# Optimization experiments

Hardware: AMD Instinct MI355X
Metric: run time of the kernel (lower is better)

## Reference

```python
import jax, jax.numpy as jnp
import numpy as np

H = 16   # num_heads
K = 2    # top_k experts per token


def _layer_norm(x, g, b, eps=1e-5):
    mu = jnp.mean(x, axis=-1, keepdims=True)
    var = jnp.mean(jnp.square(x - mu), axis=-1, keepdims=True)
    return (x - mu) * jax.lax.rsqrt(var + eps) * g + b


def setup_inputs() -> dict:
    key = jax.random.key(0)
    ks = jax.random.split(key, 8)
    B, S, D, E = 2, 2048, 1024, 8
    sc = 0.02
    return {
        "x": jax.random.normal(ks[0], (B, S, D), jnp.float32),
        "wq": jax.random.normal(ks[1], (D, D), jnp.float32) * sc,
        "wk": jax.random.normal(ks[2], (D, D), jnp.float32) * sc,
        "wv": jax.random.normal(ks[3], (D, D), jnp.float32) * sc,
        "wo": jax.random.normal(ks[4], (D, D), jnp.float32) * sc,
        "ln1_g": jnp.ones((D,), jnp.float32),
        "ln1_b": jnp.zeros((D,), jnp.float32),
        "ln2_g": jnp.ones((D,), jnp.float32),
        "ln2_b": jnp.zeros((D,), jnp.float32),
        "router_w": jax.random.normal(ks[5], (E, D), jnp.float32) * sc,
        "expert_w": jax.random.normal(ks[6], (E, D, D), jnp.float32) * sc,
    }


def reference(x, wq, wk, wv, wo, ln1_g, ln1_b, ln2_g, ln2_b, router_w, expert_w):
    B, S, D = x.shape
    E = expert_w.shape[0]
    hd = D // H

    # ---- attention sublayer: x = x + attn(norm1(x)) ----
    h = _layer_norm(x, ln1_g, ln1_b)
    q = (h @ wq.T).reshape(B, S, H, hd).transpose(0, 2, 1, 3)  # bhsd
    k = (h @ wk.T).reshape(B, S, H, hd).transpose(0, 2, 1, 3)
    v = (h @ wv.T).reshape(B, S, H, hd).transpose(0, 2, 1, 3)
    scores = jnp.einsum("bhqd,bhkd->bhqk", q, k) / jnp.sqrt(jnp.float32(hd))
    causal = jnp.tril(jnp.ones((S, S), dtype=bool))
    scores = jnp.where(causal, scores, jnp.finfo(scores.dtype).min)
    probs = jax.nn.softmax(scores, axis=-1)
    attn = jnp.einsum("bhqk,bhkd->bhqd", probs, v)
    attn = attn.transpose(0, 2, 1, 3).reshape(B, S, D) @ wo.T
    x = x + attn

    # ---- MoE sublayer: x = x + moe(norm2(x)) ----
    h2 = _layer_norm(x, ln2_g, ln2_b)
    logits = jnp.einsum("bsd,ed->bse", h2, router_w)          # [B,S,E]
    top_logits, top_ids = jax.lax.top_k(logits, K)            # [B,S,K]
    gates = jax.nn.softmax(top_logits, axis=-1)               # [B,S,K]
    # dense combine weights over experts (E is small): sum_k gate_k * onehot(id_k)
    combine = jnp.sum(jax.nn.one_hot(top_ids, E, dtype=h2.dtype) * gates[..., None], axis=-2)  # [B,S,E]
    # per-token matvec with expert weights: token @ W_e.T for each expert, then weighted sum
    y = jnp.einsum("bsd,eod->bseo", h2, expert_w)             # [B,S,E,D]
    moe_out = jnp.einsum("bse,bseo->bso", combine, y)
    return x + moe_out
```

## Files before the change

kernel.cpp:

```cpp
#include <hip/hip_runtime.h>
#include <hip/hip_bf16.h>
#include <cstdint>


typedef __bf16 bf16;
typedef __bf16 bf16x8 __attribute__((ext_vector_type(8)));
typedef __bf16 bf16x4 __attribute__((ext_vector_type(4)));
typedef float f32x4 __attribute__((ext_vector_type(4)));
typedef float f32x16 __attribute__((ext_vector_type(16)));

#define MFMA(a, b, c) __builtin_amdgcn_mfma_f32_16x16x32_bf16(a, b, c, 0, 0, 0)
#define MFMA32(a, b, c) __builtin_amdgcn_mfma_f32_32x32x16_bf16(a, b, c, 0, 0, 0)

__device__ __forceinline__ void gld16(void* lds, const void* g) {
  __builtin_amdgcn_global_load_lds(
      (const __attribute__((address_space(1))) void*)g,
      (__attribute__((address_space(3))) void*)lds, 16, 0, 0);
}

__global__ void prep_weights(const float* __restrict__ wq, const float* __restrict__ wk,
                             const float* __restrict__ wv, const float* __restrict__ wo,
                             const float* __restrict__ expw,
                             bf16* __restrict__ wqh, bf16* __restrict__ wql,
                             bf16* __restrict__ wkh, bf16* __restrict__ wkl,
                             bf16* __restrict__ wvh,
                             bf16* __restrict__ woh, bf16* __restrict__ wol,
                             bf16* __restrict__ ewh) {
  int bid = blockIdx.x;
  if (bid < 4096) {
    int wsel = bid >> 10;
    const float* src = wsel == 0 ? wq : wsel == 1 ? wk : wsel == 2 ? wv : wo;
    bf16* hi = wsel == 0 ? wqh : wsel == 1 ? wkh : wsel == 2 ? wvh : woh;
    bf16* lo = wsel == 0 ? wql : wsel == 1 ? wkl : wsel == 2 ? (bf16*)nullptr : wol;
    int i = ((bid & 1023) * 256 + threadIdx.x) * 4;
    float4 v = *(const float4*)(src + i);
    float a[4] = {v.x, v.y, v.z, v.w};
#pragma unroll
    for (int j = 0; j < 4; j++) {
      bf16 h = (bf16)a[j];
      hi[i + j] = h;
      if (wsel != 2) lo[i + j] = (bf16)(a[j] - (float)h);
    }
  } else {
    int i = ((bid - 4096) * 256 + threadIdx.x) * 4;
    float4 v = *(const float4*)(expw + i);
    ewh[i] = (bf16)v.x; ewh[i + 1] = (bf16)v.y;
    ewh[i + 2] = (bf16)v.z; ewh[i + 3] = (bf16)v.w;
  }
}

__global__ void ln_split(const float* __restrict__ x, const float* __restrict__ g,
                         const float* __restrict__ b, bf16* __restrict__ hi,
                         bf16* __restrict__ lo) {
  int tok = blockIdx.x, t = threadIdx.x;
  float4 v = ((const float4*)(x + (size_t)tok * 1024))[t];
  float s = v.x + v.y + v.z + v.w;
  float ss = v.x * v.x + v.y * v.y + v.z * v.z + v.w * v.w;
#pragma unroll
  for (int o = 1; o < 64; o <<= 1) { s += __shfl_xor(s, o); ss += __shfl_xor(ss, o); }
  __shared__ float red[8];
  int w = t >> 6, lane = t & 63;
  if (lane == 0) { red[w] = s; red[4 + w] = ss; }
  __syncthreads();
  s = red[0] + red[1] + red[2] + red[3];
  ss = red[4] + red[5] + red[6] + red[7];
  float mu = s * (1.f / 1024.f);
  float rstd = rsqrtf(ss * (1.f / 1024.f) - mu * mu + 1e-5f);
  float4 gv = ((const float4*)g)[t], bv = ((const float4*)b)[t];
  float y[4] = {(v.x - mu) * rstd * gv.x + bv.x, (v.y - mu) * rstd * gv.y + bv.y,
                (v.z - mu) * rstd * gv.z + bv.z, (v.w - mu) * rstd * gv.w + bv.w};
  size_t o = (size_t)tok * 1024 + t * 4;
#pragma unroll
  for (int j = 0; j < 4; j++) {
    bf16 h = (bf16)y[j];
    hi[o + j] = h;
    lo[o + j] = (bf16)(y[j] - (float)h);
  }
}

__global__ void ln2route(const float* __restrict__ x0,
                         const float* __restrict__ P0, const float* __restrict__ P1,
                         const float* __restrict__ g, const float* __restrict__ b,
                         const float* __restrict__ rw, float* __restrict__ outp,
                         bf16* __restrict__ h2h, int* __restrict__ eid,
                         float2* __restrict__ gout) {
  int tok = blockIdx.x, t = threadIdx.x;
  float4 xv = ((const float4*)(x0 + (size_t)tok * 1024))[t];
  float4 p0 = ((const float4*)(P0 + (size_t)tok * 1024))[t];
  float4 p1 = ((const float4*)(P1 + (size_t)tok * 1024))[t];
  float4 v;
  v.x = xv.x + p0.x + p1.x;
  v.y = xv.y + p0.y + p1.y;
  v.z = xv.z + p0.z + p1.z;
  v.w = xv.w + p0.w + p1.w;
  ((float4*)(outp + (size_t)tok * 1024))[t] = v;
  float s = v.x + v.y + v.z + v.w;
  float ss = v.x * v.x + v.y * v.y + v.z * v.z + v.w * v.w;
#pragma unroll
  for (int o = 1; o < 64; o <<= 1) { s += __shfl_xor(s, o); ss += __shfl_xor(ss, o); }
  __shared__ float red[8];
  __shared__ float h2s[1024];
  __shared__ float lg[8];
  int w = t >> 6, lane = t & 63;
  if (lane == 0) { red[w] = s; red[4 + w] = ss; }
  __syncthreads();
  s = red[0] + red[1] + red[2] + red[3];
  ss = red[4] + red[5] + red[6] + red[7];
  float mu = s * (1.f / 1024.f);
  float rstd = rsqrtf(ss * (1.f / 1024.f) - mu * mu + 1e-5f);
  float4 gv = ((const float4*)g)[t], bv = ((const float4*)b)[t];
  float4 y;
  y.x = (v.x - mu) * rstd * gv.x + bv.x;
  y.y = (v.y - mu) * rstd * gv.y + bv.y;
  y.z = (v.z - mu) * rstd * gv.z + bv.z;
  y.w = (v.w - mu) * rstd * gv.w + bv.w;
  ((float4*)h2s)[t] = y;
  size_t o = (size_t)tok * 1024 + t * 4;
  h2h[o] = (bf16)y.x; h2h[o + 1] = (bf16)y.y;
  h2h[o + 2] = (bf16)y.z; h2h[o + 3] = (bf16)y.w;
  __syncthreads();
  float a0 = 0.f, a1 = 0.f;
  const float4* r0 = (const float4*)(rw + (2 * w) * 1024);
  const float4* r1 = (const float4*)(rw + (2 * w + 1) * 1024);
#pragma unroll
  for (int it = 0; it < 4; it++) {
    float4 xv2 = ((const float4*)h2s)[lane + 64 * it];
    float4 w0 = r0[lane + 64 * it];
    float4 w1 = r1[lane + 64 * it];
    a0 += xv2.x * w0.x + xv2.y * w0.y + xv2.z * w0.z + xv2.w * w0.w;
    a1 += xv2.x * w1.x + xv2.y * w1.y + xv2.z * w1.z + xv2.w * w1.w;
  }
#pragma unroll
  for (int o2 = 1; o2 < 64; o2 <<= 1) {
    a0 += __shfl_xor(a0, o2);
    a1 += __shfl_xor(a1, o2);
  }
  if (lane == 0) { lg[2 * w] = a0; lg[2 * w + 1] = a1; }
  __syncthreads();
  if (t == 0) {
    int i0 = 0; float l0 = lg[0];
#pragma unroll
    for (int e = 1; e < 8; e++) if (lg[e] > l0) { l0 = lg[e]; i0 = e; }
    int i1 = -1; float l1 = -3e38f;
#pragma unroll
    for (int e = 0; e < 8; e++) if (e != i0 && lg[e] > l1) { l1 = lg[e]; i1 = e; }
    float e1 = __expf(l1 - l0);
    float den = 1.f + e1;
    eid[tok] = i0 | (i1 << 4);
    gout[tok] = make_float2(1.f / den, e1 / den);
  }
}

__global__ void build_lists(const int* __restrict__ eid,
                            const float2* __restrict__ gv,
                            int* __restrict__ tlist, float* __restrict__ glist,
                            int* __restrict__ cnt) {
  int e = blockIdx.x, t = threadIdx.x;
  int lane = t & 63, w = t >> 6;
  __shared__ int wt[4];
  int base = 0;
  for (int c = 0; c < 16; c++) {
    int tok = c * 256 + t;
    int pair = eid[tok];
    int e0 = pair & 15, e1 = pair >> 4;
    bool p = (e0 == e) || (e1 == e);
    float2 g2 = gv[tok];
    float gate = (e0 == e) ? g2.x : g2.y;
    unsigned long long m = __ballot(p);
    int rank = __popcll(m & ((1ull << lane) - 1ull));
    if (lane == 0) wt[w] = __popcll(m);
    __syncthreads();
    int off = base;
    for (int i = 0; i < w; i++) off += wt[i];
    if (p) {
      tlist[e * 4096 + off + rank] = tok;
      glist[e * 4096 + off + rank] = gate;
    }
    base += wt[0] + wt[1] + wt[2] + wt[3];
    __syncthreads();
  }
  if (t == 0) cnt[e] = base;
  int pad = (base + 127) & ~127;
  if (pad > 4096) pad = 4096;
  for (int i = base + t; i < pad; i += 256) {
    tlist[e * 4096 + i] = 0;
    glist[e * 4096 + i] = 0.f;
  }
}

__device__ __forceinline__ void gemm_core_split(
    const bf16* __restrict__ Ah, const bf16* __restrict__ Al,
    const bf16* __restrict__ Bh, const bf16* __restrict__ Bl, int m0, int n0,
    f32x4 (&acc)[4][4]) {
  __shared__ __align__(16) bf16 As_h[4096], As_l[4096], Bs_h[4096], Bs_l[4096];
  int t = threadIdx.x, lane = t & 63, w = t >> 6;
  int i0 = t, i1 = t + 256;
  const bf16* a0h = Ah + (size_t)(m0 + (i0 >> 2)) * 1024 + (i0 & 3) * 8;
  const bf16* a1h = Ah + (size_t)(m0 + (i1 >> 2)) * 1024 + (i1 & 3) * 8;
  const bf16* a0l = Al + (size_t)(m0 + (i0 >> 2)) * 1024 + (i0 & 3) * 8;
  const bf16* a1l = Al + (size_t)(m0 + (i1 >> 2)) * 1024 + (i1 & 3) * 8;
  const bf16* b0h = Bh + (size_t)(n0 + (i0 >> 2)) * 1024 + (i0 & 3) * 8;
  const bf16* b1h = Bh + (size_t)(n0 + (i1 >> 2)) * 1024 + (i1 & 3) * 8;
  const bf16* b0l = Bl + (size_t)(n0 + (i0 >> 2)) * 1024 + (i0 & 3) * 8;
  const bf16* b1l = Bl + (size_t)(n0 + (i1 >> 2)) * 1024 + (i1 & 3) * 8;
  int wm = (w >> 1) * 64, wn = (w & 1) * 64;
  int lr = lane & 15, lq = lane >> 4;
  for (int k0 = 0; k0 < 1024; k0 += 32) {
    __syncthreads();
    gld16(&As_h[i0 * 8], a0h + k0); gld16(&As_h[i1 * 8], a1h + k0);
    gld16(&As_l[i0 * 8], a0l + k0); gld16(&As_l[i1 * 8], a1l + k0);
    gld16(&Bs_h[i0 * 8], b0h + k0); gld16(&Bs_h[i1 * 8], b1h + k0);
    gld16(&Bs_l[i0 * 8], b0l + k0); gld16(&Bs_l[i1 * 8], b1l + k0);
    __syncthreads();
    bf16x8 ah[4], al4[4], bh[4], bl4[4];
#pragma unroll
    for (int i = 0; i < 4; i++) {
      ah[i]  = *(const bf16x8*)&As_h[(wm + i * 16 + lr) * 32 + lq * 8];
      al4[i] = *(const bf16x8*)&As_l[(wm + i * 16 + lr) * 32 + lq * 8];
      bh[i]  = *(const bf16x8*)&Bs_h[(wn + i * 16 + lr) * 32 + lq * 8];
      bl4[i] = *(const bf16x8*)&Bs_l[(wn + i * 16 + lr) * 32 + lq * 8];
    }
#pragma unroll
    for (int i = 0; i < 4; i++)
#pragma unroll
      for (int j = 0; j < 4; j++) {
        f32x4 c = acc[i][j];
        c = MFMA(ah[i], bh[j], c);
        c = MFMA(ah[i], bl4[j], c);
        c = MFMA(al4[i], bh[j], c);
        acc[i][j] = c;
      }
  }
}

__global__ __launch_bounds__(256, 3) void gemm_qkv(
    const bf16* __restrict__ hh, const bf16* __restrict__ hl,
    const bf16* __restrict__ wqh, const bf16* __restrict__ wql,
    const bf16* __restrict__ wkh, const bf16* __restrict__ wkl,
    const bf16* __restrict__ wvh,
    bf16* __restrict__ qh, bf16* __restrict__ ql, bf16* __restrict__ kh,
    bf16* __restrict__ kl, bf16* __restrict__ vth) {
  int n0 = blockIdx.x * 128, m0 = blockIdx.y * 128, z = blockIdx.z;
  int t = threadIdx.x, lane = t & 63, w = t >> 6;
  int wm = (w >> 1) * 64, wn = (w & 1) * 64, lr = lane & 15, lq = lane >> 4;
  if (z < 2) {
    const bf16* Bh = z ? wkh : wqh;
    const bf16* Bl = z ? wkl : wql;
    f32x4 acc[4][4];
#pragma unroll
    for (int i = 0; i < 4; i++)
#pragma unroll
      for (int j = 0; j < 4; j++) acc[i][j] = (f32x4){0.f, 0.f, 0.f, 0.f};
    gemm_core_split(hh, hl, Bh, Bl, m0, n0, acc);
    bf16* Oh = z ? kh : qh;
    bf16* Ol = z ? kl : ql;
    float scale = z ? 1.0f : (0.125f * 1.44269504f);
#pragma unroll
    for (int i = 0; i < 4; i++)
#pragma unroll
      for (int j = 0; j < 4; j++)
#pragma unroll
        for (int r = 0; r < 4; r++) {
          size_t row = m0 + wm + i * 16 + lq * 4 + r;
          int col = n0 + wn + j * 16 + lr;
          float v = acc[i][j][r] * scale;
          bf16 h = (bf16)v;
          Oh[row * 1024 + col] = h;
          Ol[row * 1024 + col] = (bf16)(v - (float)h);
        }
  } else {
    __shared__ __align__(16) bf16 As[4096], Bs[4096];
    int i0 = t, i1 = t + 256;
    const bf16* a0 = hh + (size_t)(m0 + (i0 >> 2)) * 1024 + (i0 & 3) * 8;
    const bf16* a1 = hh + (size_t)(m0 + (i1 >> 2)) * 1024 + (i1 & 3) * 8;
    const bf16* b0 = wvh + (size_t)(n0 + (i0 >> 2)) * 1024 + (i0 & 3) * 8;
    const bf16* b1 = wvh + (size_t)(n0 + (i1 >> 2)) * 1024 + (i1 & 3) * 8;
    f32x4 acc[4][4];
#pragma unroll
    for (int i = 0; i < 4; i++)
#pragma unroll
      for (int j = 0; j < 4; j++) acc[i][j] = (f32x4){0.f, 0.f, 0.f, 0.f};
    for (int k0 = 0; k0 < 1024; k0 += 32) {
      __syncthreads();
      gld16(&As[i0 * 8], a0 + k0); gld16(&As[i1 * 8], a1 + k0);
      gld16(&Bs[i0 * 8], b0 + k0); gld16(&Bs[i1 * 8], b1 + k0);
      __syncthreads();
      bf16x8 af[4], bfr[4];
#pragma unroll
      for (int i = 0; i < 4; i++) {
        af[i] = *(const bf16x8*)&As[(wm + i * 16 + lr) * 32 + lq * 8];
        bfr[i] = *(const bf16x8*)&Bs[(wn + i * 16 + lr) * 32 + lq * 8];
      }
#pragma unroll
      for (int i = 0; i < 4; i++)
#pragma unroll
        for (int j = 0; j < 4; j++) acc[i][j] = MFMA(af[i], bfr[j], acc[i][j]);
    }
    int bb = m0 >> 11;
    int srow0 = m0 & 2047;
#pragma unroll
    for (int i = 0; i < 4; i++)
#pragma unroll
      for (int j = 0; j < 4; j++) {
        int col = n0 + wn + j * 16 + lr;
        int head = col >> 6, d = col & 63;
        int s = srow0 + wm + i * 16 + lq * 4;
        int ss = (s & ~63) | (((((s >> 2) & 15)) ^ (d & 15)) << 2);
        bf16x4 hv;
#pragma unroll
        for (int r = 0; r < 4; r++) hv[r] = (bf16)acc[i][j][r];
        size_t off = ((size_t)((bb * 16 + head) * 64 + d)) * 2048 + ss;
        *(bf16x4*)(vth + off) = hv;
      }
  }
}

__global__ __launch_bounds__(256, 2) void gemm_wo(
    const float* __restrict__ Oacc, const float* __restrict__ Lacc,
    const bf16* __restrict__ bh, const bf16* __restrict__ bl,
    float* __restrict__ P0, float* __restrict__ P1) {
  int n0 = blockIdx.x * 128, m0 = blockIdx.y * 128, z = blockIdx.z;
  float* P = z ? P1 : P0;
  int kb = z * 512;
  __shared__ __align__(16) bf16 As_h[4096], As_l[4096], Bs_h[4096], Bs_l[4096];
  int t = threadIdx.x, lane = t & 63, w = t >> 6;
  int i0 = t, i1 = t + 256;
  int row0 = m0 + (i0 >> 2), row1 = m0 + (i1 >> 2);
  const float* a0 = Oacc + (size_t)row0 * 1024 + (i0 & 3) * 8;
  const float* a1 = Oacc + (size_t)row1 * 1024 + (i1 & 3) * 8;
  const bf16* b0h = bh + (size_t)(n0 + (i0 >> 2)) * 1024 + (i0 & 3) * 8;
  const bf16* b1h = bh + (size_t)(n0 + (i1 >> 2)) * 1024 + (i1 & 3) * 8;
  const bf16* b0l = bl + (size_t)(n0 + (i0 >> 2)) * 1024 + (i0 & 3) * 8;
  const bf16* b1l = bl + (size_t)(n0 + (i1 >> 2)) * 1024 + (i1 & 3) * 8;
  int wm = (w >> 1) * 64, wn = (w & 1) * 64;
  int lr = lane & 15, lq = lane >> 4;
  f32x4 acc[4][4];
#pragma unroll
  for (int i = 0; i < 4; i++)
#pragma unroll
    for (int j = 0; j < 4; j++) acc[i][j] = (f32x4){0.f, 0.f, 0.f, 0.f};
  for (int k0 = kb; k0 < kb + 512; k0 += 32) {
    __syncthreads();
    gld16(&Bs_h[i0 * 8], b0h + k0); gld16(&Bs_h[i1 * 8], b1h + k0);
    gld16(&Bs_l[i0 * 8], b0l + k0); gld16(&Bs_l[i1 * 8], b1l + k0);
    int hd = k0 >> 6;
    float linv0 = 1.f / Lacc[row0 * 16 + hd];
    float linv1 = 1.f / Lacc[row1 * 16 + hd];
    float4 va0 = *(const float4*)(a0 + k0);
    float4 vb0 = *(const float4*)(a0 + k0 + 4);
    float4 va1 = *(const float4*)(a1 + k0);
    float4 vb1 = *(const float4*)(a1 + k0 + 4);
    float f0[8] = {va0.x, va0.y, va0.z, va0.w, vb0.x, vb0.y, vb0.z, vb0.w};
    float f1[8] = {va1.x, va1.y, va1.z, va1.w, vb1.x, vb1.y, vb1.z, vb1.w};
    bf16x8 h0, l0, h1, l1;
#pragma unroll
    for (int j = 0; j < 8; j++) {
      float x0 = f0[j] * linv0;
      bf16 hh0 = (bf16)x0;
      h0[j] = hh0; l0[j] = (bf16)(x0 - (float)hh0);
      float x1 = f1[j] * linv1;
      bf16 hh1 = (bf16)x1;
      h1[j] = hh1; l1[j] = (bf16)(x1 - (float)hh1);
    }
    *(bf16x8*)&As_h[i0 * 8] = h0; *(bf16x8*)&As_l[i0 * 8] = l0;
    *(bf16x8*)&As_h[i1 * 8] = h1; *(bf16x8*)&As_l[i1 * 8] = l1;
    __syncthreads();
    bf16x8 ah[4], al4[4], bhf[4], bl4[4];
#pragma unroll
    for (int i = 0; i < 4; i++) {
      ah[i]  = *(const bf16x8*)&As_h[(wm + i * 16 + lr) * 32 + lq * 8];
      al4[i] = *(const bf16x8*)&As_l[(wm + i * 16 + lr) * 32 + lq * 8];
      bhf[i] = *(const bf16x8*)&Bs_h[(wn + i * 16 + lr) * 32 + lq * 8];
      bl4[i] = *(const bf16x8*)&Bs_l[(wn + i * 16 + lr) * 32 + lq * 8];
    }
#pragma unroll
    for (int i = 0; i < 4; i++)
#pragma unroll
      for (int j = 0; j < 4; j++) {
        f32x4 c = acc[i][j];
        c = MFMA(ah[i], bhf[j], c);
        c = MFMA(ah[i], bl4[j], c);
        c = MFMA(al4[i], bhf[j], c);
        acc[i][j] = c;
      }
  }
#pragma unroll
  for (int i = 0; i < 4; i++)
#pragma unroll
    for (int j = 0; j < 4; j++)
#pragma unroll
      for (int r = 0; r < 4; r++) {
        size_t row = m0 + wm + i * 16 + lq * 4 + r;
        int col = n0 + wn + j * 16 + lr;
        P[row * 1024 + col] = acc[i][j][r];
      }
}

__device__ __forceinline__ f32x16 qk_subtile(
    const bf16* __restrict__ Ks, const bf16* __restrict__ Kls, int keyr, int l5,
    const bf16x8 (&qfh)[4], const bf16x8 (&qfl)[4]) {
  f32x16 sA, sB;
#pragma unroll
  for (int r = 0; r < 16; r++) { sA[r] = 0.f; sB[r] = 0.f; }
#pragma unroll
  for (int c = 0; c < 4; c++) {
    int dg = ((2 * c + l5) ^ (keyr & 7)) * 8;
    bf16x8 kv = *(const bf16x8*)&Ks[keyr * 64 + dg];
    bf16x8 km = *(const bf16x8*)&Kls[keyr * 64 + dg];
    if (c < 2) {
      sA = MFMA32(kv, qfh[c], sA);
      sA = MFMA32(kv, qfl[c], sA);
      sA = MFMA32(km, qfh[c], sA);
    } else {
      sB = MFMA32(kv, qfh[c], sB);
      sB = MFMA32(kv, qfl[c], sB);
      sB = MFMA32(km, qfh[c], sB);
    }
  }
  return sA + sB;
}

__device__ __forceinline__ void exp_pack_pv(
    f32x16 sc, bool maskt, int kb0, int qg, int ktile,
    float& lsum, f32x16& O0, f32x16& O1,
    const bf16* __restrict__ Vs, int l31, int l5) {
  float pvv[16];
#pragma unroll
  for (int r = 0; r < 16; r++) {
    int cst = (r & 3) + 8 * (r >> 2);
    float sv = sc[r];
    if (maskt && (kb0 + cst > qg)) sv = -30000.f;
    float p = __builtin_amdgcn_exp2f(sv);
    pvv[r] = p;
    lsum += p;
  }
  uint32_t hw[4][2], lw[4][2];
#pragma unroll
  for (int o = 0; o < 4; o++)
#pragma unroll
    for (int j = 0; j < 2; j++) {
      int ra = 4 * o + 2 * j;
      bf16 h0 = (bf16)pvv[ra], h1 = (bf16)pvv[ra + 1];
      union { bf16 h[2]; uint32_t u; } ph, pl;
      ph.h[0] = h0; ph.h[1] = h1;
      pl.h[0] = (bf16)(pvv[ra] - (float)h0);
      pl.h[1] = (bf16)(pvv[ra + 1] - (float)h1);
      hw[o][j] = ph.u;
      lw[o][j] = pl.u;
    }
#pragma unroll
  for (int c2 = 0; c2 < 2; c2++) {
    union { uint32_t u[4]; bf16x8 v; } pa, plo;
    pa.u[0] = hw[2 * c2][0];     pa.u[1] = hw[2 * c2][1];
    pa.u[2] = hw[2 * c2 + 1][0]; pa.u[3] = hw[2 * c2 + 1][1];
    plo.u[0] = lw[2 * c2][0];     plo.u[1] = lw[2 * c2][1];
    plo.u[2] = lw[2 * c2 + 1][0]; plo.u[3] = lw[2 * c2 + 1][1];
    __builtin_amdgcn_s_setprio(1);
#pragma unroll
    for (int dtile = 0; dtile < 2; dtile++) {
      int d = dtile * 32 + l31;
      int pqA = ((8 * ktile + 4 * c2 + l5) ^ (d & 15)) * 4;
      union { bf16x4 q[2]; bf16x8 v; } vbu;
      vbu.q[0] = *(const bf16x4*)&Vs[d * 64 + pqA];
      vbu.q[1] = *(const bf16x4*)&Vs[d * 64 + (pqA ^ 8)];
      if (dtile == 0) {
        O0 = MFMA32(pa.v, vbu.v, O0);
        O0 = MFMA32(plo.v, vbu.v, O0);
      } else {
        O1 = MFMA32(pa.v, vbu.v, O1);
        O1 = MFMA32(plo.v, vbu.v, O1);
      }
    }
    __builtin_amdgcn_s_setprio(0);
  }
}

__global__ __launch_bounds__(256, 3) void attn_fused(
    const bf16* __restrict__ qh, const bf16* __restrict__ ql,
    const bf16* __restrict__ kh, const bf16* __restrict__ kl,
    const bf16* __restrict__ vth,
    float* __restrict__ O_acc, float* __restrict__ L_acc) {
  const int S = 2048, D = 1024;
  static const unsigned char QTt[40] = {
      15, 15, 15, 15, 14, 14, 14, 13, 13, 13, 12, 12, 12, 11, 11, 11,
      10, 10, 9, 9, 8, 8, 7, 7, 6, 5, 4, 3,
      14, 10, 6, 2, 13, 9, 5, 1, 12, 8, 4, 0};
  static const unsigned char C0t[40] = {
      0, 8, 16, 24, 0, 8, 16, 0, 8, 16, 0, 8, 16, 0, 8, 16,
      0, 8, 0, 8, 0, 8, 0, 8, 0, 0, 0, 0,
      24, 16, 8, 0, 24, 16, 8, 0, 24, 16, 8, 0};
  static const unsigned char C1t[40] = {
      8, 16, 24, 32, 8, 16, 24, 8, 16, 24, 8, 16, 24, 8, 16, 24,
      8, 16, 8, 16, 8, 16, 8, 16, 8, 8, 8, 8,
      30, 22, 14, 6, 28, 20, 12, 4, 26, 18, 10, 2};
  int y = blockIdx.y;
  int qt = QTt[y];
  int tile0 = C0t[y], tile1 = C1t[y];
  int hb = blockIdx.x;
  int head = hb & 15, b = hb >> 4;
  int qb = qt * 128;
  int t = threadIdx.x, lane = t & 63, w = t >> 6;
  int l31 = lane & 31, l5 = lane >> 5;
  int base = b * S, hcol = head * 64;

  __shared__ __align__(16) bf16 Kh_s[2][4096], Kl_s[2][4096];
  __shared__ __align__(16) bf16 Vh_s[2][4096];

  bf16x8 qfh[4], qfl[4];
  {
    const bf16* p1 = qh + (size_t)(base + qb + w * 32 + l31) * D + hcol + l5 * 8;
    const bf16* p2 = ql + (size_t)(base + qb + w * 32 + l31) * D + hcol + l5 * 8;
#pragma unroll
    for (int c = 0; c < 4; c++) {
      qfh[c] = *(const bf16x8*)(p1 + 16 * c);
      qfl[c] = *(const bf16x8*)(p2 + 16 * c);
    }
  }
  f32x16 O0, O1;
  float lsum = 0.f;
#pragma unroll
  for (int r = 0; r < 16; r++) { O0[r] = 0.f; O1[r] = 0.f; }

  int r0 = t >> 3, p0 = t & 7;
  int g0 = p0 ^ (r0 & 7);
  const bf16* k0hp = kh + (size_t)(base + r0) * D + hcol + g0 * 8;
  const bf16* k1hp = kh + (size_t)(base + 32 + r0) * D + hcol + g0 * 8;
  const bf16* k0lp = kl + (size_t)(base + r0) * D + hcol + g0 * 8;
  const bf16* k1lp = kl + (size_t)(base + 32 + r0) * D + hcol + g0 * 8;
  const bf16* v0hp = vth + (size_t)(hb * 64 + r0) * 2048 + p0 * 8;
  const bf16* v1hp = vth + (size_t)(hb * 64 + 32 + r0) * 2048 + p0 * 8;

  int qwmin = qb + w * 32;

#define STAGE(kts, bb) do { \
    gld16(&Kh_s[bb][t * 8], k0hp + (size_t)(kts) * D); \
    gld16(&Kh_s[bb][2048 + t * 8], k1hp + (size_t)(kts) * D); \
    gld16(&Kl_s[bb][t * 8], k0lp + (size_t)(kts) * D); \
    gld16(&Kl_s[bb][2048 + t * 8], k1lp + (size_t)(kts) * D); \
    gld16(&Vh_s[bb][t * 8], v0hp + (kts)); \
    gld16(&Vh_s[bb][2048 + t * 8], v1hp + (kts)); \
  } while (0)

  STAGE(tile0 * 64, tile0 & 1);
  __syncthreads();

  for (int ti = tile0; ti < tile1; ++ti) {
    int kt = ti * 64;
    int bb = ti & 1;
    if (ti + 1 < tile1) STAGE((ti + 1) * 64, bb ^ 1);
    const bf16* Ks = &Kh_s[bb][0];
    const bf16* Kls = &Kl_s[bb][0];
    const bf16* Vs = &Vh_s[bb][0];
    if (kt + 64 <= qb) {
      __builtin_amdgcn_s_setprio(1);
      f32x16 sc0 = qk_subtile(Ks, Kls, l31, l5, qfh, qfl);
      f32x16 sc1 = qk_subtile(Ks, Kls, 32 + l31, l5, qfh, qfl);
      __builtin_amdgcn_s_setprio(0);
      exp_pack_pv(sc0, false, 0, 0, 0, lsum, O0, O1, Vs, l31, l5);
      exp_pack_pv(sc1, false, 0, 0, 1, lsum, O0, O1, Vs, l31, l5);
    } else if (kt <= qwmin + 31) {
      bool skip1 = (kt + 32 > qwmin + 31);
#pragma unroll
      for (int ktile = 0; ktile < 2; ktile++) {
        if (ktile == 1 && skip1) break;
        bool maskt = (kt + 32 * ktile + 31 > qwmin);
        __builtin_amdgcn_s_setprio(1);
        f32x16 sc = qk_subtile(Ks, Kls, ktile * 32 + l31, l5, qfh, qfl);
        __builtin_amdgcn_s_setprio(0);
        int kb0 = kt + 32 * ktile + 4 * l5;
        int qg = qwmin + l31;
        exp_pack_pv(sc, maskt, kb0, qg, ktile, lsum, O0, O1, Vs, l31, l5);
      }
    }
    __syncthreads();
  }
#undef STAGE
  if (tile0 * 64 <= qwmin + 31) {
    float ltot = lsum + __shfl_xor(lsum, 32);
    if (l5 == 0) {
      size_t tokq = (size_t)(base + qb + w * 32 + l31);
      atomicAdd(&L_acc[tokq * 16 + head], ltot);
    }
#pragma unroll
    for (int r = 0; r < 16; r++) {
      int qlocal = (r & 3) + 8 * (r >> 2) + 4 * l5;
      size_t tok = (size_t)(base + qb + w * 32 + qlocal);
      atomicAdd(&O_acc[tok * 1024 + hcol + l31], O0[r]);
      atomicAdd(&O_acc[tok * 1024 + hcol + 32 + l31], O1[r]);
    }
  }
}

__global__ __launch_bounds__(256, 2) void gemm_moe(
    const bf16* __restrict__ A, const bf16* __restrict__ W,
    const int* __restrict__ tlist, const float* __restrict__ glist,
    const int* __restrict__ cnt, float* __restrict__ outp) {
  int e = blockIdx.z;
  int count = cnt[e];
  int m0 = blockIdx.y * 128;
  if (m0 >= count) return;
  int n0 = blockIdx.x * 128;
  const int* tl = tlist + e * 4096;
  const bf16* B = W + (size_t)e * 1024 * 1024;
  __shared__ __align__(16) bf16 As[4096], Bs[4096];
  int t = threadIdx.x, lane = t & 63, w = t >> 6;
  int i0 = t, i1 = t + 256;
  int ra = tl[m0 + (i0 >> 2)], rb = tl[m0 + (i1 >> 2)];
  const bf16* a0 = A + (size_t)ra * 1024 + (i0 & 3) * 8;
  const bf16* a1 = A + (size_t)rb * 1024 + (i1 & 3) * 8;
  const bf16* b0 = B + (size_t)(n0 + (i0 >> 2)) * 1024 + (i0 & 3) * 8;
  const bf16* b1 = B + (size_t)(n0 + (i1 >> 2)) * 1024 + (i1 & 3) * 8;
  int wm = (w >> 1) * 64, wn = (w & 1) * 64, lr = lane & 15, lq = lane >> 4;
  f32x4 acc[4][4];
#pragma unroll
  for (int i = 0; i < 4; i++)
#pragma unroll
    for (int j = 0; j < 4; j++) acc[i][j] = (f32x4){0.f, 0.f, 0.f, 0.f};
  for (int k0 = 0; k0 < 1024; k0 += 32) {
    __syncthreads();
    gld16(&As[i0 * 8], a0 + k0); gld16(&As[i1 * 8], a1 + k0);
    gld16(&Bs[i0 * 8], b0 + k0); gld16(&Bs[i1 * 8], b1 + k0);
    __syncthreads();
    bf16x8 af[4], bfr[4];
#pragma unroll
    for (int i = 0; i < 4; i++) {
      af[i] = *(const bf16x8*)&As[(wm + i * 16 + lr) * 32 + lq * 8];
      bfr[i] = *(const bf16x8*)&Bs[(wn + i * 16 + lr) * 32 + lq * 8];
    }
#pragma unroll
    for (int i = 0; i < 4; i++)
#pragma unroll
      for (int j = 0; j < 4; j++) acc[i][j] = MFMA(af[i], bfr[j], acc[i][j]);
  }
#pragma unroll
  for (int i = 0; i < 4; i++)
#pragma unroll
    for (int r = 0; r < 4; r++) {
      int slot = m0 + wm + i * 16 + lq * 4 + r;
      if (slot < count) {
        int tok = tl[slot];
        float gte = glist[e * 4096 + slot];
#pragma unroll
        for (int j = 0; j < 4; j++) {
          int col = n0 + wn + j * 16 + lr;
          atomicAdd(&outp[(size_t)tok * 1024 + col], gte * acc[i][j][r]);
        }
      }
    }
}

extern "C" void kernel_launch(void* const* d_in, const int* in_sizes, int n_in,
                              void* d_out, int out_size, void* d_ws, size_t ws_size,
                              hipStream_t stream) {
  (void)in_sizes; (void)n_in; (void)out_size; (void)ws_size;
  const float* x    = (const float*)d_in[0];
  const float* wq   = (const float*)d_in[1];
  const float* wk   = (const float*)d_in[2];
  const float* wv   = (const float*)d_in[3];
  const float* wo   = (const float*)d_in[4];
  const float* ln1g = (const float*)d_in[5];
  const float* ln1b = (const float*)d_in[6];
  const float* ln2g = (const float*)d_in[7];
  const float* ln2b = (const float*)d_in[8];
  const float* rw   = (const float*)d_in[9];
  const float* expw = (const float*)d_in[10];
  float* out = (float*)d_out;

  char* p = (char*)d_ws;
  auto take = [&](size_t bytes) -> char* {
    char* r = p;
    p += (bytes + 255) & ~(size_t)255;
    return r;
  };
  const size_t ND2 = 4096ull * 1024 * 2;
  const size_t WD2 = 1024ull * 1024 * 2;
  bf16* h_hi = (bf16*)take(ND2); bf16* h_lo = (bf16*)take(ND2);
  bf16* wqh = (bf16*)take(WD2); bf16* wql = (bf16*)take(WD2);
  bf16* wkh = (bf16*)take(WD2); bf16* wkl = (bf16*)take(WD2);
  bf16* wvh = (bf16*)take(WD2);
  bf16* woh = (bf16*)take(WD2); bf16* wol = (bf16*)take(WD2);
  bf16* q_hi = (bf16*)take(ND2); bf16* q_lo = (bf16*)take(ND2);
  bf16* k_hi = (bf16*)take(ND2); bf16* k_lo = (bf16*)take(ND2);
  bf16* vt_hi = (bf16*)take(ND2);
  bf16* h2h  = (bf16*)take(ND2);
  bf16* ewh  = (bf16*)take(8ull * 1024 * 1024 * 2);
  int*   tlist  = (int*)take(8ull * 4096 * 4);
  float* glist  = (float*)take(8ull * 4096 * 4);
  int*   cnt    = (int*)take(64);
  int*   reid   = (int*)take(4096 * 4);
  float2* rg    = (float2*)take(4096 * 8);
  float* O_acc  = (float*)take(4096ull * 1024 * 4);
  float* L_acc  = (float*)take(4096ull * 16 * 4);
  float* P0 = (float*)q_hi;
  float* P1 = (float*)k_hi;

  hipMemsetAsync(O_acc, 0, 4096ull * 1024 * 4 + 4096ull * 16 * 4, stream);
  prep_weights<<<12288, 256, 0, stream>>>(wq, wk, wv, wo, expw, wqh, wql, wkh,
                                          wkl, wvh, woh, wol, ewh);
  ln_split<<<4096, 256, 0, stream>>>(x, ln1g, ln1b, h_hi, h_lo);
  gemm_qkv<<<dim3(8, 32, 3), 256, 0, stream>>>(h_hi, h_lo, wqh, wql, wkh, wkl,
                                               wvh, q_hi, q_lo, k_hi, k_lo,
                                               vt_hi);
  attn_fused<<<dim3(32, 40), 256, 0, stream>>>(q_hi, q_lo, k_hi, k_lo, vt_hi,
                                               O_acc, L_acc);
  gemm_wo<<<dim3(8, 32, 2), 256, 0, stream>>>(O_acc, L_acc, woh, wol, P0, P1);
  ln2route<<<4096, 256, 0, stream>>>(x, P0, P1, ln2g, ln2b, rw, out, h2h,
                                     reid, rg);
  build_lists<<<8, 256, 0, stream>>>(reid, rg, tlist, glist, cnt);
  gemm_moe<<<dim3(8, 32, 8), 256, 0, stream>>>(h2h, ewh, tlist, glist, cnt,
                                               out);
}
```

Before: 374.2 us.

## Single-buffer attention LDS for occupancy and split MoE GEMM along K

The attention kernel drops its double-buffered K/V shared-memory staging in favour of a single buffer with syncs around each load. This halves LDS use so more blocks can be resident (launch bound raised to 5), at the cost of losing the overlap between prefetch and compute. The MoE GEMM is split into two K halves across a doubled grid, relying on atomic accumulation into the output, which gives more parallel blocks and higher occupancy but adds more atomic traffic.

```diff
diff --git a/kernel.cpp b/kernel.cpp
--- a/kernel.cpp
+++ b/kernel.cpp
@@ -475,7 +475,7 @@
   }
 }
 
-__global__ __launch_bounds__(256, 3) void attn_fused(
+__global__ __launch_bounds__(256, 5) void attn_fused(
     const bf16* __restrict__ qh, const bf16* __restrict__ ql,
     const bf16* __restrict__ kh, const bf16* __restrict__ kl,
     const bf16* __restrict__ vth,
@@ -503,8 +503,8 @@
   int l31 = lane & 31, l5 = lane >> 5;
   int base = b * S, hcol = head * 64;
 
-  __shared__ __align__(16) bf16 Kh_s[2][4096], Kl_s[2][4096];
-  __shared__ __align__(16) bf16 Vh_s[2][4096];
+  __shared__ __align__(16) bf16 Kh_s[4096], Kl_s[4096];
+  __shared__ __align__(16) bf16 Vh_s[4096];
 
   bf16x8 qfh[4], qfl[4];
   {
@@ -532,32 +532,27 @@
 
   int qwmin = qb + w * 32;
 
-#define STAGE(kts, bb) do { \
-    gld16(&Kh_s[bb][t * 8], k0hp + (size_t)(kts) * D); \
-    gld16(&Kh_s[bb][2048 + t * 8], k1hp + (size_t)(kts) * D); \
-    gld16(&Kl_s[bb][t * 8], k0lp + (size_t)(kts) * D); \
-    gld16(&Kl_s[bb][2048 + t * 8], k1lp + (size_t)(kts) * D); \
-    gld16(&Vh_s[bb][t * 8], v0hp + (kts)); \
-    gld16(&Vh_s[bb][2048 + t * 8], v1hp + (kts)); \
+#define STAGE(kts) do { \
+    gld16(&Kh_s[t * 8], k0hp + (size_t)(kts) * D); \
+    gld16(&Kh_s[2048 + t * 8], k1hp + (size_t)(kts) * D); \
+    gld16(&Kl_s[t * 8], k0lp + (size_t)(kts) * D); \
+    gld16(&Kl_s[2048 + t * 8], k1lp + (size_t)(kts) * D); \
+    gld16(&Vh_s[t * 8], v0hp + (kts)); \
+    gld16(&Vh_s[2048 + t * 8], v1hp + (kts)); \
   } while (0)
-
-  STAGE(tile0 * 64, tile0 & 1);
-  __syncthreads();
 
   for (int ti = tile0; ti < tile1; ++ti) {
     int kt = ti * 64;
-    int bb = ti & 1;
-    if (ti + 1 < tile1) STAGE((ti + 1) * 64, bb ^ 1);
-    const bf16* Ks = &Kh_s[bb][0];
-    const bf16* Kls = &Kl_s[bb][0];
-    const bf16* Vs = &Vh_s[bb][0];
+    __syncthreads();
+    STAGE(kt);
+    __syncthreads();
     if (kt + 64 <= qb) {
       __builtin_amdgcn_s_setprio(1);
-      f32x16 sc0 = qk_subtile(Ks, Kls, l31, l5, qfh, qfl);
-      f32x16 sc1 = qk_subtile(Ks, Kls, 32 + l31, l5, qfh, qfl);
+      f32x16 sc0 = qk_subtile(Kh_s, Kl_s, l31, l5, qfh, qfl);
+      f32x16 sc1 = qk_subtile(Kh_s, Kl_s, 32 + l31, l5, qfh, qfl);
       __builtin_amdgcn_s_setprio(0);
-      exp_pack_pv(sc0, false, 0, 0, 0, lsum, O0, O1, Vs, l31, l5);
-      exp_pack_pv(sc1, false, 0, 0, 1, lsum, O0, O1, Vs, l31, l5);
+      exp_pack_pv(sc0, false, 0, 0, 0, lsum, O0, O1, Vh_s, l31, l5);
+      exp_pack_pv(sc1, false, 0, 0, 1, lsum, O0, O1, Vh_s, l31, l5);
     } else if (kt <= qwmin + 31) {
       bool skip1 = (kt + 32 > qwmin + 31);
 #pragma unroll
@@ -565,14 +560,13 @@
         if (ktile == 1 && skip1) break;
         bool maskt = (kt + 32 * ktile + 31 > qwmin);
         __builtin_amdgcn_s_setprio(1);
-        f32x16 sc = qk_subtile(Ks, Kls, ktile * 32 + l31, l5, qfh, qfl);
+        f32x16 sc = qk_subtile(Kh_s, Kl_s, ktile * 32 + l31, l5, qfh, qfl);
         __builtin_amdgcn_s_setprio(0);
         int kb0 = kt + 32 * ktile + 4 * l5;
         int qg = qwmin + l31;
-        exp_pack_pv(sc, maskt, kb0, qg, ktile, lsum, O0, O1, Vs, l31, l5);
+        exp_pack_pv(sc, maskt, kb0, qg, ktile, lsum, O0, O1, Vh_s, l31, l5);
       }
     }
-    __syncthreads();
   }
 #undef STAGE
   if (tile0 * 64 <= qwmin + 31) {
@@ -591,11 +585,13 @@
   }
 }
 
-__global__ __launch_bounds__(256, 2) void gemm_moe(
+__global__ __launch_bounds__(256, 4) void gemm_moe(
     const bf16* __restrict__ A, const bf16* __restrict__ W,
     const int* __restrict__ tlist, const float* __restrict__ glist,
     const int* __restrict__ cnt, float* __restrict__ outp) {
-  int e = blockIdx.z;
+  int ez = blockIdx.z;
+  int e = ez >> 1;
+  int kb = (ez & 1) * 512;
   int count = cnt[e];
   int m0 = blockIdx.y * 128;
   if (m0 >= count) return;
@@ -616,7 +612,7 @@
   for (int i = 0; i < 4; i++)
 #pragma unroll
     for (int j = 0; j < 4; j++) acc[i][j] = (f32x4){0.f, 0.f, 0.f, 0.f};
-  for (int k0 = 0; k0 < 1024; k0 += 32) {
+  for (int k0 = kb; k0 < kb + 512; k0 += 32) {
     __syncthreads();
     gld16(&As[i0 * 8], a0 + k0); gld16(&As[i1 * 8], a1 + k0);
     gld16(&Bs[i0 * 8], b0 + k0); gld16(&Bs[i1 * 8], b1 + k0);
@@ -707,6 +703,6 @@
   ln2route<<<4096, 256, 0, stream>>>(x, P0, P1, ln2g, ln2b, rw, out, h2h,
                                      reid, rg);
   build_lists<<<8, 256, 0, stream>>>(reid, rg, tlist, glist, cnt);
-  gemm_moe<<<dim3(8, 32, 8), 256, 0, stream>>>(h2h, ewh, tlist, glist, cnt,
-                                               out);
-}
+  gemm_moe<<<dim3(8, 32, 16), 256, 0, stream>>>(h2h, ewh, tlist, glist, cnt,
+                                                out);
+}
```

New measurement: 621.0 us. 1.66x slower.
